# Performance work log

Measured on AMD Instinct MI355X. Metric: run time of the kernel, lower is better.

The kernel has to match this reference:

```python
import jax, jax.numpy as jnp
import numpy as np

N_NODES = 50000
N_EDGES = 600000
DIM = 128
VOCAB = 512
PAD_ID = 0
LN_EPS = 1e-5


def setup_inputs() -> dict:
    key = jax.random.key(0)
    ks = jax.random.split(key, 8)
    node_ids = jax.random.randint(ks[0], (N_NODES,), 0, VOCAB, dtype=jnp.int32)
    edge_index = jax.random.randint(ks[1], (2, N_EDGES), 0, N_NODES, dtype=jnp.int32)
    edge_weight = jax.random.uniform(ks[2], (N_EDGES,), dtype=jnp.float32)
    # embedding with padding row zeroed (padding_idx semantics)
    emb = jax.random.normal(ks[3], (VOCAB, DIM), dtype=jnp.float32) * 0.05
    emb = emb.at[PAD_ID].set(0.0)
    s = 1.0 / np.sqrt(DIM)
    W1 = jax.random.normal(ks[4], (DIM, DIM), dtype=jnp.float32) * s
    b1 = jnp.zeros((DIM,), jnp.float32)
    W2 = jax.random.normal(ks[5], (DIM, DIM), dtype=jnp.float32) * s
    b2 = jnp.zeros((DIM,), jnp.float32)
    return {
        "node_ids": node_ids, "edge_index": edge_index, "edge_weight": edge_weight,
        "emb": emb, "W1": W1, "b1": b1, "W2": W2, "b2": b2,
        "gamma1": jnp.ones((DIM,), jnp.float32), "beta1": jnp.zeros((DIM,), jnp.float32),
        "gamma2": jnp.ones((DIM,), jnp.float32), "beta2": jnp.zeros((DIM,), jnp.float32),
    }


def _gcn_conv(x, row, col, ew, W, b, n_nodes):
    """PyG GCNConv: normalize=True, add_self_loops=True, improved=False.
    Aggregation j->i: edge (row=src j, col=dst i)."""
    h = x @ W  # [N, out]
    # add self loops with weight 1
    loop = jnp.arange(n_nodes, dtype=row.dtype)
    row_f = jnp.concatenate([row, loop])
    col_f = jnp.concatenate([col, loop])
    ew_f = jnp.concatenate([ew, jnp.ones((n_nodes,), ew.dtype)])
    # symmetric degree normalization (deg over destination index)
    deg = jax.ops.segment_sum(ew_f, col_f, num_segments=n_nodes)
    dis = jnp.where(deg > 0, jax.lax.rsqrt(jnp.maximum(deg, 1e-12)), 0.0)
    norm = dis[row_f] * ew_f * dis[col_f]  # [E+N]
    msg = norm[:, None] * h[row_f]  # gather + scale  [E+N, out]
    out = jax.ops.segment_sum(msg, col_f, num_segments=n_nodes)  # scatter-add
    return out + b


def _layer_norm(x, gamma, beta):
    mu = jnp.mean(x, axis=-1, keepdims=True)
    var = jnp.mean(jnp.square(x - mu), axis=-1, keepdims=True)
    return (x - mu) * jax.lax.rsqrt(var + LN_EPS) * gamma + beta


def reference(node_ids, edge_index, edge_weight, emb, W1, b1, W2, b2,
              gamma1, beta1, gamma2, beta2):
    row, col = edge_index[0], edge_index[1]
    x = emb[node_ids]  # [N, D]
    x1 = _gcn_conv(x, row, col, edge_weight, W1, b1, N_NODES)
    x = _layer_norm(x + x1, gamma1, beta1)  # dropout is identity in eval
    x2 = _gcn_conv(x, row, col, edge_weight, W2, b2, N_NODES)
    x = _layer_norm(x + x2, gamma2, beta2)
    return x
```

## Files before the change

kernel.cpp:

```cpp
#include <hip/hip_runtime.h>

#define N_NODES 50000
#define N_EDGES 600000
#define DIM     128
#define VOCAB   512
#define LN_EPS  1e-5f
#define FIX20   1048576.0f
#define WSC     65535.0f
#define BCAP    64

typedef unsigned int uint;
typedef unsigned long long ull;
typedef unsigned short ushort;
typedef __attribute__((ext_vector_type(8))) short s8v;
typedef __attribute__((ext_vector_type(4))) float f4v;
typedef __attribute__((ext_vector_type(4))) int   i4v;
typedef __attribute__((ext_vector_type(4))) float fv4;
typedef __attribute__((ext_vector_type(2))) float f2v;

__device__ __forceinline__ uint f2bf(float f) {
    uint u = __float_as_uint(f);
    return (u + 0x7fffu + ((u >> 16) & 1u)) >> 16;
}
__device__ __forceinline__ float bf_lo(uint p) { return __uint_as_float(p << 16); }
__device__ __forceinline__ float bf_hi(uint p) { return __uint_as_float(p & 0xffff0000u); }
__device__ __forceinline__ float dis_of(uint pv) {
    return rsqrtf(1.0f + (float)(pv & 0x03ffffffu) * (1.0f / FIX20));
}

__global__ __launch_bounds__(256) void deg_mm1_kernel(
        const int* __restrict__ ei, const float* __restrict__ ew,
        uint* pack, uint* __restrict__ epack, int E,
        const float* __restrict__ X, const float* __restrict__ W,
        uint* __restrict__ Hb, int M,
        const float* __restrict__ W2, ushort* __restrict__ Wp) {
    __shared__ float Wt[32 * 128];
    __shared__ float Xt[64 * 36];
    int tid = threadIdx.x;
    int nbDeg = (E / 4 + 255) / 256;
    int nmm = (M + 63) / 64;
    if ((int)blockIdx.x < nbDeg) {
        int e0 = (blockIdx.x * 256 + tid) * 4;
        if (e0 >= E) return;
        i4v s4 = __builtin_nontemporal_load((const i4v*)(ei + e0));
        i4v c4 = __builtin_nontemporal_load((const i4v*)(ei + E + e0));
        fv4 w4 = __builtin_nontemporal_load((const fv4*)(ew + e0));
        int   s[4] = {s4.x, s4.y, s4.z, s4.w};
        int   c[4] = {c4.x, c4.y, c4.z, c4.w};
        float w[4] = {w4.x, w4.y, w4.z, w4.w};
        uint r[4];
        #pragma unroll
        for (int k = 0; k < 4; k++) {
            uint a = (1u << 26) | (uint)__float2int_rn(w[k] * FIX20);
            r[k] = atomicAdd(&pack[c[k]], a);
        }
        #pragma unroll
        for (int k = 0; k < 4; k++) {
            uint rk = r[k] >> 26;
            uint wq = (uint)__float2int_rn(w[k] * WSC);
            epack[(size_t)c[k] * BCAP + rk] = (uint)s[k] | (wq << 16);
        }
        return;
    }
    if ((int)blockIdx.x >= nbDeg + nmm) {
        int o = (blockIdx.x - nbDeg - nmm) * 256 + tid;
        int j = o & 7, lane = (o >> 3) & 63, chunk = o >> 9;
        int kc = chunk & 3, nc = chunk >> 2;
        int k = kc * 32 + (lane >> 4) * 8 + j;
        int n = nc * 16 + (lane & 15);
        Wp[o] = (ushort)f2bf(W2[k * 128 + n]);
        return;
    }
    int bx = blockIdx.x - nbDeg;
    int tx = tid & 31, ty = tid >> 5;
    int r0 = bx * 64;
    float acc[8][4];
    #pragma unroll
    for (int j = 0; j < 8; j++)
        #pragma unroll
        for (int c = 0; c < 4; c++) acc[j][c] = 0.f;

    for (int kb = 0; kb < 128; kb += 32) {
        __syncthreads();
        #pragma unroll
        for (int q = 0; q < 4; q++) {
            int f = q * 256 + tid;
            ((float4*)Wt)[f] = *(const float4*)(W + kb * 128 + f * 4);
        }
        #pragma unroll
        for (int q = 0; q < 2; q++) {
            int f = q * 256 + tid;
            int row = f >> 3, cs = f & 7;
            int gr = r0 + row;
            float4 xv = make_float4(0.f, 0.f, 0.f, 0.f);
            if (gr < M) xv = *(const float4*)(X + (size_t)gr * 128 + kb + cs * 4);
            *(float4*)(Xt + row * 36 + cs * 4) = xv;
        }
        __syncthreads();
        #pragma unroll
        for (int k = 0; k < 32; k += 4) {
            float wv[4][4];
            #pragma unroll
            for (int kk = 0; kk < 4; kk++) {
                float4 t4 = *(const float4*)(Wt + (k + kk) * 128 + tx * 4);
                wv[kk][0] = t4.x; wv[kk][1] = t4.y; wv[kk][2] = t4.z; wv[kk][3] = t4.w;
            }
            #pragma unroll
            for (int j = 0; j < 8; j++) {
                float4 xv = *(const float4*)(Xt + (ty * 8 + j) * 36 + k);
                float xs[4] = {xv.x, xv.y, xv.z, xv.w};
                #pragma unroll
                for (int kk = 0; kk < 4; kk++)
                    #pragma unroll
                    for (int c = 0; c < 4; c++)
                        acc[j][c] = fmaf(xs[kk], wv[kk][c], acc[j][c]);
            }
        }
    }
    #pragma unroll
    for (int j = 0; j < 8; j++) {
        int gr = r0 + ty * 8 + j;
        if (gr < M) {
            uint p0 = f2bf(acc[j][0]) | (f2bf(acc[j][1]) << 16);
            uint p1 = f2bf(acc[j][2]) | (f2bf(acc[j][3]) << 16);
            ((uint2*)Hb)[(size_t)gr * 32 + tx] = make_uint2(p0, p1);
        }
    }
}

__global__ __launch_bounds__(256) void mm2_mfma(const uint* __restrict__ Xb,
                                                const ushort* __restrict__ Wp,
                                                const uint* __restrict__ pack,
                                                char* __restrict__ H8,
                                                float* __restrict__ rowscale, int M) {
    int wid = (blockIdx.x * 256 + threadIdx.x) >> 6;
    int lane = threadIdx.x & 63;
    int r0 = wid * 16;
    if (r0 >= M) return;
    int quad = lane >> 4, lo = lane & 15;
    const uint* xrow = Xb + (size_t)(r0 + lo) * 64 + quad * 4;
    s8v a[4];
    #pragma unroll
    for (int kc = 0; kc < 4; kc++) a[kc] = *(const s8v*)(xrow + kc * 16);
    f4v acc[8];
    #pragma unroll
    for (int nc = 0; nc < 8; nc++) {
        acc[nc] = (f4v){0.f, 0.f, 0.f, 0.f};
        #pragma unroll
        for (int kc = 0; kc < 4; kc++) {
            s8v b = *(const s8v*)(Wp + (size_t)((nc * 4 + kc) * 64 + lane) * 8);
            acc[nc] = __builtin_amdgcn_mfma_f32_16x16x32_bf16(a[kc], b, acc[nc], 0, 0, 0);
        }
    }
    float m[4];
    #pragma unroll
    for (int r = 0; r < 4; r++) {
        m[r] = 0.f;
        #pragma unroll
        for (int nc = 0; nc < 8; nc++) m[r] = fmaxf(m[r], fabsf(acc[nc][r]));
    }
    #pragma unroll
    for (int o = 1; o <= 8; o <<= 1)
        #pragma unroll
        for (int r = 0; r < 4; r++) m[r] = fmaxf(m[r], __shfl_xor(m[r], o, 64));
    #pragma unroll
    for (int r = 0; r < 4; r++) {
        float inv = (m[r] > 0.f) ? 127.0f / m[r] : 0.f;
        if (lo == 0) {
            int rr = r0 + quad * 4 + r;
            rowscale[rr] = m[r] * (1.0f / 127.0f) * dis_of(pack[rr]);
        }
        char* hp = H8 + (size_t)(r0 + quad * 4 + r) * 128 + lo;
        #pragma unroll
        for (int nc = 0; nc < 8; nc++)
            hp[nc * 16] = (char)__float2int_rn(acc[nc][r] * inv);
    }
}

template<bool RESID_BF, bool OUT_BF, bool GI8>
__global__ __launch_bounds__(256) void agg_ln(const uint* __restrict__ pack,
                                              const uint* __restrict__ epack,
                                              const void* __restrict__ hb,
                                              const float* __restrict__ rowscale,
                                              const int* __restrict__ nid,
                                              const void* __restrict__ resid,
                                              const float* __restrict__ bias,
                                              const float* __restrict__ gamma,
                                              const float* __restrict__ beta,
                                              void* __restrict__ out, int n) {
    int i = (blockIdx.x * 256 + threadIdx.x) >> 6;
    int lane = threadIdx.x & 63;
    if (i >= n) return;
    int iw = __builtin_amdgcn_readfirstlane(i);
    uint pv = pack[iw];
    int deg = (int)(pv >> 26);
    float dl = dis_of(pv);
    int hri = GI8 ? iw : nid[iw];
    float slo, shi;
    if (GI8) {
        uint ps = ((const ushort*)hb)[(size_t)hri * 64 + lane];
        float sc = rowscale[hri];
        slo = sc * (float)(signed char)(ps & 0xffu);
        shi = sc * (float)(signed char)(ps >> 8);
    } else {
        uint ps = ((const uint*)hb)[(size_t)hri * 64 + lane];
        slo = bf_lo(ps); shi = bf_hi(ps);
    }
    float sx[4] = {GI8 ? slo : dl * slo, 0.f, 0.f, 0.f};
    float sy[4] = {GI8 ? shi : dl * shi, 0.f, 0.f, 0.f};
    const uint* ep = epack + (size_t)iw * BCAP;
    for (int j = 0; j < deg; j += 8) {
        uint er[8];
        #pragma unroll
        for (int k = 0; k < 8; k++) {
            int idx = (j + k < deg) ? j + k : deg - 1;
            er[k] = ep[idx];
        }
        uint qv[8];
        float sc[8];
        #pragma unroll
        for (int k = 0; k < 8; k++) {
            uint src = er[k] & 0xffffu;
            if (GI8) {
                qv[k] = ((const ushort*)hb)[(size_t)src * 64 + lane];
                sc[k] = rowscale[src];
            } else {
                size_t row = (uint)nid[src];
                qv[k] = ((const uint*)hb)[row * 64 + lane];
                sc[k] = (float)(pack[src] & 0x03ffffffu);
            }
        }
        #pragma unroll
        for (int k = 0; k < 8; k++) {
            float w = (j + k < deg) ? (float)(er[k] >> 16) * (1.0f / WSC) : 0.f;
            float lo, hi;
            if (GI8) {
                w *= sc[k];
                lo = (float)(signed char)(qv[k] & 0xffu);
                hi = (float)(signed char)(qv[k] >> 8);
            } else {
                w *= rsqrtf(1.0f + sc[k] * (1.0f / FIX20));
                lo = bf_lo(qv[k]); hi = bf_hi(qv[k]);
            }
            sx[k & 3] += w * lo;
            sy[k & 3] += w * hi;
        }
    }
    float acc0 = (sx[0] + sx[1]) + (sx[2] + sx[3]);
    float acc1 = (sy[0] + sy[1]) + (sy[2] + sy[3]);
    float2 xr;
    if (RESID_BF) {
        uint pr = __builtin_nontemporal_load((const uint*)resid + (size_t)hri * 64 + lane);
        xr = make_float2(bf_lo(pr), bf_hi(pr));
    } else {
        xr = ((const float2*)resid)[(size_t)hri * 64 + lane];
    }
    float2 bi = ((const float2*)bias)[lane];
    float v0 = xr.x + dl * acc0 + bi.x;
    float v1 = xr.y + dl * acc1 + bi.y;
    float s1 = v0 + v1, s2 = v0 * v0 + v1 * v1;
    #pragma unroll
    for (int o = 32; o > 0; o >>= 1) {
        s1 += __shfl_xor(s1, o, 64);
        s2 += __shfl_xor(s2, o, 64);
    }
    float mu   = s1 * (1.0f / DIM);
    float var  = s2 * (1.0f / DIM) - mu * mu;
    float rstd = rsqrtf(var + LN_EPS);
    float2 ga = ((const float2*)gamma)[lane];
    float2 be = ((const float2*)beta)[lane];
    float o0 = (v0 - mu) * rstd * ga.x + be.x;
    float o1 = (v1 - mu) * rstd * ga.y + be.y;
    if (OUT_BF) {
        __builtin_nontemporal_store(f2bf(o0) | (f2bf(o1) << 16),
                                    (uint*)out + (size_t)i * 64 + lane);
    } else {
        f2v ov = {o0, o1};
        __builtin_nontemporal_store(ov, (f2v*)((float2*)out + (size_t)i * 64 + lane));
    }
}

extern "C" void kernel_launch(void* const* d_in, const int* in_sizes, int n_in,
                              void* d_out, int out_size, void* d_ws, size_t ws_size,
                              hipStream_t stream) {
    const int*   node_ids = (const int*)  d_in[0];
    const int*   ei       = (const int*)  d_in[1];
    const float* ew       = (const float*)d_in[2];
    const float* emb      = (const float*)d_in[3];
    const float* W1       = (const float*)d_in[4];
    const float* b1       = (const float*)d_in[5];
    const float* W2       = (const float*)d_in[6];
    const float* b2       = (const float*)d_in[7];
    const float* g1       = (const float*)d_in[8];
    const float* be1      = (const float*)d_in[9];
    const float* g2       = (const float*)d_in[10];
    const float* be2      = (const float*)d_in[11];
    float* out = (float*)d_out;

    char* p = (char*)d_ws;
    auto alloc = [&](size_t bytes) {
        char* r = p;
        p += (bytes + 255) & ~(size_t)255;
        return r;
    };
    char*   h8      = (char*)  alloc((size_t)N_NODES * DIM);
    float*  rsc     = (float*) alloc((size_t)N_NODES * 4);
    uint*   x1b     = (uint*)  alloc((size_t)N_NODES * 64 * 4);
    uint*   hembB   = (uint*)  alloc((size_t)VOCAB * 64 * 4);
    ushort* Wp      = (ushort*)alloc((size_t)128 * 128 * 2);
    uint*   pack    = (uint*)  alloc((size_t)N_NODES * 4);
    uint*   epack   = (uint*)  alloc((size_t)N_NODES * BCAP * 4);

    int nbDeg = (N_EDGES / 4 + 255) / 256;
    int nmm = (VOCAB + 63) / 64;

    (void)hipMemsetAsync(pack, 0, (size_t)N_NODES * 4, stream);
    deg_mm1_kernel<<<nbDeg + nmm + 64, 256, 0, stream>>>(
        ei, ew, pack, epack, N_EDGES, emb, W1, hembB, VOCAB, W2, Wp);

    agg_ln<false, true, false><<<(N_NODES + 3) / 4, 256, 0, stream>>>(
        pack, epack, hembB, nullptr, node_ids, emb, b1, g1, be1, x1b, N_NODES);

    mm2_mfma<<<(N_NODES / 16 + 3) / 4, 256, 0, stream>>>(x1b, Wp, pack, h8, rsc, N_NODES);
    agg_ln<true, false, true><<<(N_NODES + 3) / 4, 256, 0, stream>>>(
        pack, epack, h8, rsc, nullptr, x1b, b2, g2, be2, out, N_NODES);
}
```

Baseline: 216.1 us.

## Interleave degree pack with node ids and widen neighbor loop to vector loads

Stores each node's packed degree word alongside its vocab id in one uint2 array, filled by extra tail blocks of the first kernel. The first aggregation then fetches both with one 8-byte gather instead of two dependent scattered loads. The neighbor loop now reads 16 edge records per iteration with four uint4 loads instead of eight scalar clamped loads, which adds memory-level parallelism but raises register pressure. Padded slots read past deg inside the per-node bucket and are masked, but the memset zeroes a larger array.

```diff
diff --git a/kernel.cpp b/kernel.cpp
--- a/kernel.cpp
+++ b/kernel.cpp
@@ -30,7 +30,7 @@
 
 __global__ __launch_bounds__(256) void deg_mm1_kernel(
         const int* __restrict__ ei, const float* __restrict__ ew,
-        uint* pack, uint* __restrict__ epack, int E,
+        uint2* pairN, const int* __restrict__ nid, uint* __restrict__ epack, int E,
         const float* __restrict__ X, const float* __restrict__ W,
         uint* __restrict__ Hb, int M,
         const float* __restrict__ W2, ushort* __restrict__ Wp) {
@@ -52,7 +52,7 @@
         #pragma unroll
         for (int k = 0; k < 4; k++) {
             uint a = (1u << 26) | (uint)__float2int_rn(w[k] * FIX20);
-            r[k] = atomicAdd(&pack[c[k]], a);
+            r[k] = atomicAdd(&((uint*)pairN)[2 * (size_t)c[k]], a);
         }
         #pragma unroll
         for (int k = 0; k < 4; k++) {
@@ -64,11 +64,16 @@
     }
     if ((int)blockIdx.x >= nbDeg + nmm) {
         int o = (blockIdx.x - nbDeg - nmm) * 256 + tid;
-        int j = o & 7, lane = (o >> 3) & 63, chunk = o >> 9;
-        int kc = chunk & 3, nc = chunk >> 2;
-        int k = kc * 32 + (lane >> 4) * 8 + j;
-        int n = nc * 16 + (lane & 15);
-        Wp[o] = (ushort)f2bf(W2[k * 128 + n]);
+        if (o < 16384) {
+            int j = o & 7, lane = (o >> 3) & 63, chunk = o >> 9;
+            int kc = chunk & 3, nc = chunk >> 2;
+            int k = kc * 32 + (lane >> 4) * 8 + j;
+            int n = nc * 16 + (lane & 15);
+            Wp[o] = (ushort)f2bf(W2[k * 128 + n]);
+        } else {
+            int i = o - 16384;
+            if (i < N_NODES) ((uint*)pairN)[2 * (size_t)i + 1] = (uint)nid[i];
+        }
         return;
     }
     int bx = blockIdx.x - nbDeg;
@@ -130,7 +135,7 @@
 
 __global__ __launch_bounds__(256) void mm2_mfma(const uint* __restrict__ Xb,
                                                 const ushort* __restrict__ Wp,
-                                                const uint* __restrict__ pack,
+                                                const uint2* __restrict__ pairN,
                                                 char* __restrict__ H8,
                                                 float* __restrict__ rowscale, int M) {
     int wid = (blockIdx.x * 256 + threadIdx.x) >> 6;
@@ -168,7 +173,7 @@
         float inv = (m[r] > 0.f) ? 127.0f / m[r] : 0.f;
         if (lo == 0) {
             int rr = r0 + quad * 4 + r;
-            rowscale[rr] = m[r] * (1.0f / 127.0f) * dis_of(pack[rr]);
+            rowscale[rr] = m[r] * (1.0f / 127.0f) * dis_of(pairN[rr].x);
         }
         char* hp = H8 + (size_t)(r0 + quad * 4 + r) * 128 + lo;
         #pragma unroll
@@ -178,11 +183,10 @@
 }
 
 template<bool RESID_BF, bool OUT_BF, bool GI8>
-__global__ __launch_bounds__(256) void agg_ln(const uint* __restrict__ pack,
+__global__ __launch_bounds__(256) void agg_ln(const uint2* __restrict__ pairN,
                                               const uint* __restrict__ epack,
                                               const void* __restrict__ hb,
                                               const float* __restrict__ rowscale,
-                                              const int* __restrict__ nid,
                                               const void* __restrict__ resid,
                                               const float* __restrict__ bias,
                                               const float* __restrict__ gamma,
@@ -192,16 +196,17 @@
     int lane = threadIdx.x & 63;
     if (i >= n) return;
     int iw = __builtin_amdgcn_readfirstlane(i);
-    uint pv = pack[iw];
+    uint2 pnw = pairN[iw];
+    uint pv = pnw.x;
     int deg = (int)(pv >> 26);
     float dl = dis_of(pv);
-    int hri = GI8 ? iw : nid[iw];
+    int hri = GI8 ? iw : (int)pnw.y;
     float slo, shi;
     if (GI8) {
         uint ps = ((const ushort*)hb)[(size_t)hri * 64 + lane];
-        float sc = rowscale[hri];
-        slo = sc * (float)(signed char)(ps & 0xffu);
-        shi = sc * (float)(signed char)(ps >> 8);
+        float sc0 = rowscale[hri];
+        slo = sc0 * (float)(signed char)(ps & 0xffu);
+        shi = sc0 * (float)(signed char)(ps >> 8);
     } else {
         uint ps = ((const uint*)hb)[(size_t)hri * 64 + lane];
         slo = bf_lo(ps); shi = bf_hi(ps);
@@ -209,37 +214,51 @@
     float sx[4] = {GI8 ? slo : dl * slo, 0.f, 0.f, 0.f};
     float sy[4] = {GI8 ? shi : dl * shi, 0.f, 0.f, 0.f};
     const uint* ep = epack + (size_t)iw * BCAP;
-    for (int j = 0; j < deg; j += 8) {
-        uint er[8];
-        #pragma unroll
-        for (int k = 0; k < 8; k++) {
-            int idx = (j + k < deg) ? j + k : deg - 1;
-            er[k] = ep[idx];
-        }
-        uint qv[8];
-        float sc[8];
-        #pragma unroll
-        for (int k = 0; k < 8; k++) {
-            uint src = er[k] & 0xffffu;
-            if (GI8) {
-                qv[k] = ((const ushort*)hb)[(size_t)src * 64 + lane];
-                sc[k] = rowscale[src];
-            } else {
-                size_t row = (uint)nid[src];
-                qv[k] = ((const uint*)hb)[row * 64 + lane];
-                sc[k] = (float)(pack[src] & 0x03ffffffu);
-            }
-        }
-        #pragma unroll
-        for (int k = 0; k < 8; k++) {
-            float w = (j + k < deg) ? (float)(er[k] >> 16) * (1.0f / WSC) : 0.f;
+
+    for (int j0 = 0; j0 < deg; j0 += 16) {
+        uint4 rv0 = ((const uint4*)(ep + j0))[0];
+        uint4 rv1 = ((const uint4*)(ep + j0))[1];
+        uint4 rv2 = ((const uint4*)(ep + j0))[2];
+        uint4 rv3 = ((const uint4*)(ep + j0))[3];
+        uint rec[16] = {rv0.x, rv0.y, rv0.z, rv0.w,
+                        rv1.x, rv1.y, rv1.z, rv1.w,
+                        rv2.x, rv2.y, rv2.z, rv2.w,
+                        rv3.x, rv3.y, rv3.z, rv3.w};
+        uint src[16];
+        #pragma unroll
+        for (int k = 0; k < 16; k++)
+            src[k] = (j0 + k < deg) ? (rec[k] & 0xffffu) : 0u;
+        uint qv[16];
+        float scv[16];
+        if (GI8) {
+            #pragma unroll
+            for (int k = 0; k < 16; k++)
+                qv[k] = ((const ushort*)hb)[(size_t)src[k] * 64 + lane];
+            #pragma unroll
+            for (int k = 0; k < 16; k++)
+                scv[k] = rowscale[src[k]];
+        } else {
+            uint2 pnk[16];
+            #pragma unroll
+            for (int k = 0; k < 16; k++)
+                pnk[k] = pairN[src[k]];
+            #pragma unroll
+            for (int k = 0; k < 16; k++)
+                qv[k] = ((const uint*)hb)[(size_t)pnk[k].y * 64 + lane];
+            #pragma unroll
+            for (int k = 0; k < 16; k++)
+                scv[k] = (float)(pnk[k].x & 0x03ffffffu);
+        }
+        #pragma unroll
+        for (int k = 0; k < 16; k++) {
+            float w = (j0 + k < deg) ? (float)(rec[k] >> 16) * (1.0f / WSC) : 0.f;
             float lo, hi;
             if (GI8) {
-                w *= sc[k];
+                w *= scv[k];
                 lo = (float)(signed char)(qv[k] & 0xffu);
                 hi = (float)(signed char)(qv[k] >> 8);
             } else {
-                w *= rsqrtf(1.0f + sc[k] * (1.0f / FIX20));
+                w *= rsqrtf(1.0f + scv[k] * (1.0f / FIX20));
                 lo = bf_lo(qv[k]); hi = bf_hi(qv[k]);
             }
             sx[k & 3] += w * lo;
@@ -308,20 +327,21 @@
     uint*   x1b     = (uint*)  alloc((size_t)N_NODES * 64 * 4);
     uint*   hembB   = (uint*)  alloc((size_t)VOCAB * 64 * 4);
     ushort* Wp      = (ushort*)alloc((size_t)128 * 128 * 2);
-    uint*   pack    = (uint*)  alloc((size_t)N_NODES * 4);
+    uint2*  pairN   = (uint2*) alloc((size_t)N_NODES * 8);
     uint*   epack   = (uint*)  alloc((size_t)N_NODES * BCAP * 4);
 
     int nbDeg = (N_EDGES / 4 + 255) / 256;
     int nmm = (VOCAB + 63) / 64;
-
-    (void)hipMemsetAsync(pack, 0, (size_t)N_NODES * 4, stream);
-    deg_mm1_kernel<<<nbDeg + nmm + 64, 256, 0, stream>>>(
-        ei, ew, pack, epack, N_EDGES, emb, W1, hembB, VOCAB, W2, Wp);
+    int nTail = 64 + (N_NODES + 255) / 256;
+
+    (void)hipMemsetAsync(pairN, 0, (size_t)N_NODES * 8, stream);
+    deg_mm1_kernel<<<nbDeg + nmm + nTail, 256, 0, stream>>>(
+        ei, ew, pairN, node_ids, epack, N_EDGES, emb, W1, hembB, VOCAB, W2, Wp);
 
     agg_ln<false, true, false><<<(N_NODES + 3) / 4, 256, 0, stream>>>(
-        pack, epack, hembB, nullptr, node_ids, emb, b1, g1, be1, x1b, N_NODES);
-
-    mm2_mfma<<<(N_NODES / 16 + 3) / 4, 256, 0, stream>>>(x1b, Wp, pack, h8, rsc, N_NODES);
+        pairN, epack, hembB, nullptr, emb, b1, g1, be1, x1b, N_NODES);
+
+    mm2_mfma<<<(N_NODES / 16 + 3) / 4, 256, 0, stream>>>(x1b, Wp, pairN, h8, rsc, N_NODES);
     agg_ln<true, false, true><<<(N_NODES + 3) / 4, 256, 0, stream>>>(
-        pack, epack, h8, rsc, nullptr, x1b, b2, g2, be2, out, N_NODES);
-}
+        pairN, epack, h8, rsc, x1b, b2, g2, be2, out, N_NODES);
+}
```

After: 207.2 us. 1.04x faster.
